# Performance work log

Measured on AMD Instinct MI355X. Metric: run time of the kernel, lower is better.

## Reference

```python
import jax, jax.numpy as jnp
import numpy as np

S, B, IN, OUT = 32, 256, 1024, 1024

def setup_inputs() -> dict:
    key = jax.random.key(0)
    ks = jax.random.split(key, 7)
    return {
        "input": jax.random.normal(ks[0], (S, B, IN), dtype=jnp.float32),
        "weight_mu": jax.random.normal(ks[1], (OUT, IN), dtype=jnp.float32) * 0.1,
        "weight_rho": jax.random.normal(ks[2], (OUT, IN), dtype=jnp.float32) - 3.0,
        "bias_mu": jax.random.normal(ks[3], (OUT,), dtype=jnp.float32) * 0.1,
        "bias_rho": jax.random.normal(ks[4], (OUT,), dtype=jnp.float32) - 3.0,
        "eps_w": jax.random.normal(ks[5], (S, OUT, IN), dtype=jnp.float32),
        "eps_b": jax.random.normal(ks[6], (S, OUT), dtype=jnp.float32),
    }

def reference(input, weight_mu, weight_rho, bias_mu, bias_rho, eps_w, eps_b):
    # sigma = log(1 + exp(rho))  (softplus)
    weight_sigma = jax.nn.softplus(weight_rho)              # (out, in)
    bias_sigma = jax.nn.softplus(bias_rho)                  # (out,)
    # reparameterized samples: (S, out, in) and (S, out)
    weight = weight_mu[None, :, :] + weight_sigma[None, :, :] * eps_w
    bias = bias_mu[None, :] + bias_sigma[None, :] * eps_b
    # batch_linear: per-sample x @ W^T + b
    out = jnp.einsum('sbi,soi->sbo', input, weight) + bias[:, None, :]
    return out
```

## Files before the change

### kernel.cpp

```cpp
#include <hip/hip_runtime.h>
#include <hip/hip_bf16.h>

constexpr int kS   = 32;
constexpr int kB   = 256;
constexpr int kIN  = 1024;
constexpr int kOUT = 1024;
constexpr int BM   = 256;
constexpr int BN   = 64;
constexpr int BK   = 32;
constexpr int NT   = kIN / BK;

typedef __bf16 v8bf __attribute__((ext_vector_type(8)));
typedef float  v4f  __attribute__((ext_vector_type(4)));

__device__ __forceinline__ float softplus_f(float x) {
    return fmaxf(x, 0.0f) + log1pf(expf(-fabsf(x)));
}
__device__ __forceinline__ unsigned int bfbits(float x) {
    __bf16 h = (__bf16)x;
    unsigned short u;
    __builtin_memcpy(&u, &h, 2);
    return (unsigned int)u;
}
__device__ __forceinline__ float asf(unsigned int u) {
    float f; __builtin_memcpy(&f, &u, 4); return f;
}

__global__ void sigma_pack(const float* __restrict__ mu, const float* __restrict__ rho,
                           uint4* __restrict__ ms) {
    int gid = blockIdx.x * blockDim.x + threadIdx.x;
    float4 m = reinterpret_cast<const float4*>(mu)[gid];
    float4 r = reinterpret_cast<const float4*>(rho)[gid];
    uint4 o;
    o.x = bfbits(m.x) | (bfbits(softplus_f(r.x)) << 16);
    o.y = bfbits(m.y) | (bfbits(softplus_f(r.y)) << 16);
    o.z = bfbits(m.z) | (bfbits(softplus_f(r.z)) << 16);
    o.w = bfbits(m.w) | (bfbits(softplus_f(r.w)) << 16);
    ms[gid] = o;
}

__global__ void xcast_kernel(const float* __restrict__ X, __bf16* __restrict__ Xb) {
    size_t i = ((size_t)blockIdx.x * blockDim.x + threadIdx.x) * 8;
    float4 a = *reinterpret_cast<const float4*>(X + i);
    float4 b = *reinterpret_cast<const float4*>(X + i + 4);
    v8bf r;
    r[0] = (__bf16)a.x; r[1] = (__bf16)a.y; r[2] = (__bf16)a.z; r[3] = (__bf16)a.w;
    r[4] = (__bf16)b.x; r[5] = (__bf16)b.y; r[6] = (__bf16)b.z; r[7] = (__bf16)b.w;
    *reinterpret_cast<v8bf*>(Xb + i) = r;
}

#define GLDS16(g, l) __builtin_amdgcn_global_load_lds(                      \
    (const __attribute__((address_space(1))) void*)(g),                     \
    (__attribute__((address_space(3))) void*)(l), 16, 0, 0)

template<bool XBF>
__global__ __launch_bounds__(512, 2) void dv_main(
        const void* __restrict__ Xv,
        const unsigned int* __restrict__ MS,
        const float* __restrict__ Ew,
        const float* __restrict__ Bmu,
        const float* __restrict__ Brho,
        const float* __restrict__ Eb,
        float* __restrict__ O)
{
    __shared__ __attribute__((aligned(16))) __bf16       Xs[3][BM * BK];
    __shared__ __attribute__((aligned(16))) float        Epb[3][BN * BK];
    __shared__ __attribute__((aligned(16))) unsigned int Msb[3][BN * BK];

    const int tid = threadIdx.x, bb = blockIdx.x;
    const int xcd = bb & 7;
    const int jj  = bb >> 3;
    const int s   = (xcd << 2) | (jj & 3);
    const int o_base = (jj >> 2) * BN;

    const int lane = tid & 63, wv = tid >> 6;
    const int mwv = wv >> 1, nwv = wv & 1;
    const int lr = lane & 15, kg = lane >> 4;

    const __bf16* Xbase = (const __bf16*)Xv + (size_t)s * kB * kIN;
    const int erow = wv * 8 + (lane >> 3);
    const int ec16 = (lane & 7) ^ ((lane >> 3) & 7);
    const float*        Ebase = Ew + ((size_t)s * kOUT + o_base + erow) * kIN + ec16 * 4;
    const unsigned int* Mbase = MS + (size_t)(o_base + erow) * kIN + ec16 * 4;
    const float* Xgf = (const float*)Xv + ((size_t)s * kB + mwv * 64 + lr) * kIN + kg * 8;

    auto STAGE = [&](int t, int bf) {
        if constexpr (XBF) {
            #pragma unroll
            for (int q = 0; q < 2; ++q) {
                int row = wv * 32 + q * 16 + (lane >> 2);
                int qg  = ((lane & 3) - (row >> 2)) & 3;
                GLDS16(Xbase + (size_t)row * kIN + t * BK + qg * 8,
                       &Xs[bf][(wv * 32 + q * 16) * BK]);
            }
        }
        GLDS16(Ebase + t * BK, &Epb[bf][wv * 256]);
        GLDS16(Mbase + t * BK, &Msb[bf][wv * 256]);
    };

    v4f acc[4][2] = {};

    STAGE(0, 0);
    STAGE(1, 1);

    for (int t = 0; t < NT; ++t) {
        const int bf = t % 3;

        if (t < NT - 1) {
            if constexpr (XBF)
                asm volatile("s_waitcnt vmcnt(4) lgkmcnt(0)" ::: "memory");
            else
                asm volatile("s_waitcnt vmcnt(2) lgkmcnt(0)" ::: "memory");
        } else {
            asm volatile("s_waitcnt vmcnt(0) lgkmcnt(0)" ::: "memory");
        }
        __builtin_amdgcn_s_barrier();

        if (t + 2 < NT) STAGE(t + 2, (t + 2) % 3);

        v8bf a[4];
        if constexpr (XBF) {
            #pragma unroll
            for (int mf = 0; mf < 4; ++mf) {
                int row = mwv * 64 + mf * 16 + lr;
                int ql  = (kg + (row >> 2)) & 3;
                a[mf] = *reinterpret_cast<const v8bf*>(&Xs[bf][row * BK + ql * 8]);
            }
        } else {
            #pragma unroll
            for (int mf = 0; mf < 4; ++mf) {
                const float* xp = Xgf + (size_t)mf * 16 * kIN + t * BK;
                float4 x0 = *reinterpret_cast<const float4*>(xp);
                float4 x1 = *reinterpret_cast<const float4*>(xp + 4);
                v8bf tt;
                tt[0] = (__bf16)x0.x; tt[1] = (__bf16)x0.y;
                tt[2] = (__bf16)x0.z; tt[3] = (__bf16)x0.w;
                tt[4] = (__bf16)x1.x; tt[5] = (__bf16)x1.y;
                tt[6] = (__bf16)x1.z; tt[7] = (__bf16)x1.w;
                a[mf] = tt;
            }
        }

        v8bf b[2];
        const char* eb = (const char*)&Epb[bf][0];
        const char* mb = (const char*)&Msb[bf][0];
        #pragma unroll
        for (int nf = 0; nf < 2; ++nf) {
            int r  = nwv * 32 + nf * 16 + lr;
            int o0 = (r * 128 + kg * 32) ^ ((r & 7) << 4);
            float4 e0 = *reinterpret_cast<const float4*>(eb + o0);
            float4 e1 = *reinterpret_cast<const float4*>(eb + (o0 ^ 16));
            uint4  p0 = *reinterpret_cast<const uint4*>(mb + o0);
            uint4  p1 = *reinterpret_cast<const uint4*>(mb + (o0 ^ 16));
            b[nf][0] = (__bf16)fmaf(asf(p0.x & 0xffff0000u), e0.x, asf(p0.x << 16));
            b[nf][1] = (__bf16)fmaf(asf(p0.y & 0xffff0000u), e0.y, asf(p0.y << 16));
            b[nf][2] = (__bf16)fmaf(asf(p0.z & 0xffff0000u), e0.z, asf(p0.z << 16));
            b[nf][3] = (__bf16)fmaf(asf(p0.w & 0xffff0000u), e0.w, asf(p0.w << 16));
            b[nf][4] = (__bf16)fmaf(asf(p1.x & 0xffff0000u), e1.x, asf(p1.x << 16));
            b[nf][5] = (__bf16)fmaf(asf(p1.y & 0xffff0000u), e1.y, asf(p1.y << 16));
            b[nf][6] = (__bf16)fmaf(asf(p1.z & 0xffff0000u), e1.z, asf(p1.z << 16));
            b[nf][7] = (__bf16)fmaf(asf(p1.w & 0xffff0000u), e1.w, asf(p1.w << 16));
        }

        #pragma unroll
        for (int mf = 0; mf < 4; ++mf)
            #pragma unroll
            for (int nf = 0; nf < 2; ++nf)
                acc[mf][nf] = __builtin_amdgcn_mfma_f32_16x16x32_bf16(
                    a[mf], b[nf], acc[mf][nf], 0, 0, 0);
    }

    float bias[2];
    #pragma unroll
    for (int nf = 0; nf < 2; ++nf) {
        int o = o_base + nwv * 32 + nf * 16 + lr;
        bias[nf] = fmaf(softplus_f(Brho[o]), Eb[(size_t)s * kOUT + o], Bmu[o]);
    }
    #pragma unroll
    for (int mf = 0; mf < 4; ++mf) {
        #pragma unroll
        for (int rr = 0; rr < 4; ++rr) {
            int mrow = mwv * 64 + mf * 16 + kg * 4 + rr;
            float* orow = O + ((size_t)s * kB + mrow) * kOUT + o_base + nwv * 32;
            #pragma unroll
            for (int nf = 0; nf < 2; ++nf)
                __builtin_nontemporal_store(acc[mf][nf][rr] + bias[nf],
                                            orow + nf * 16 + lr);
        }
    }
}

extern "C" void kernel_launch(void* const* d_in, const int* in_sizes, int n_in,
                              void* d_out, int out_size, void* d_ws, size_t ws_size,
                              hipStream_t stream) {
    const float* input = (const float*)d_in[0];
    const float* w_mu  = (const float*)d_in[1];
    const float* w_rho = (const float*)d_in[2];
    const float* b_mu  = (const float*)d_in[3];
    const float* b_rho = (const float*)d_in[4];
    const float* eps_w = (const float*)d_in[5];
    const float* eps_b = (const float*)d_in[6];
    float* out = (float*)d_out;

    const size_t ms_bytes  = (size_t)kOUT * kIN * 4;
    const size_t xbf_bytes = (size_t)kS * kB * kIN * sizeof(__bf16);
    const bool use_xbf = ws_size >= ms_bytes + xbf_bytes;

    unsigned int* ms = (unsigned int*)d_ws;
    __bf16* xbf = (__bf16*)((char*)d_ws + ms_bytes);

    sigma_pack<<<dim3((kOUT * kIN) / (256 * 4)), 256, 0, stream>>>(w_mu, w_rho, (uint4*)ms);

    dim3 grid(kS * (kOUT / BN));
    if (use_xbf) {
        xcast_kernel<<<dim3((size_t)kS * kB * kIN / (256 * 8)), 256, 0, stream>>>(input, xbf);
        dv_main<true><<<grid, 512, 0, stream>>>(xbf, ms, eps_w, b_mu, b_rho, eps_b, out);
    } else {
        dv_main<false><<<grid, 512, 0, stream>>>(input, ms, eps_w, b_mu, b_rho, eps_b, out);
    }
}
```

Before: 298.0 us.

## Split weight sampling into a pre-pass producing tiled bf16 weights for GEMM

Adds a wmat kernel that computes the sampled weights mu + sigma*eps once, stored as bf16 in a pre-swizzled per-tile layout. The GEMM then loads ready bf16 weight tiles instead of fp32 eps and packed mu/sigma, removing conversion math from the inner loop, and raises occupancy to 4 blocks per SM. The cost is an extra write and read of a 64MB intermediate. A naive fallback kernel replaces the fp32-input path when workspace is insufficient.

After: 302.1 us. Within noise of the previous version (+1.4%).

```diff
diff --git a/kernel.cpp b/kernel.cpp
--- a/kernel.cpp
+++ b/kernel.cpp
@@ -5,11 +5,11 @@
 constexpr int kB   = 256;
 constexpr int kIN  = 1024;
 constexpr int kOUT = 1024;
-constexpr int BM   = 256;
 constexpr int BN   = 64;
 constexpr int BK   = 32;
 constexpr int NT   = kIN / BK;
 
+typedef __bf16 v4bf __attribute__((ext_vector_type(4)));
 typedef __bf16 v8bf __attribute__((ext_vector_type(8)));
 typedef float  v4f  __attribute__((ext_vector_type(4)));
 
@@ -49,53 +49,84 @@
     *reinterpret_cast<v8bf*>(Xb + i) = r;
 }
 
+__global__ __launch_bounds__(256, 4) void wmat(
+        const unsigned int* __restrict__ MS,
+        const float* __restrict__ Ew,
+        __bf16* __restrict__ Wp)
+{
+    const int bb  = blockIdx.x;
+    const int s   = bb & 31;
+    const int rr  = bb >> 5;
+    const int ot  = rr >> 2;
+    const int q   = rr & 3;
+    const int tid = threadIdx.x;
+
+    const float*        Eg = Ew + ((size_t)s * kOUT + ot * 64) * kIN;
+    const unsigned int* Mg = MS + (size_t)(ot * 64) * kIN;
+    char* Wt = (char*)(Wp + ((size_t)(s * 16 + ot) * NT) * 2048);
+
+    #pragma unroll 4
+    for (int i = tid; i < 16 * 256; i += 256) {
+        int row = q * 16 + (i >> 8);
+        int k   = (i & 255) * 4;
+        float4 e = *reinterpret_cast<const float4*>(Eg + (size_t)row * kIN + k);
+        uint4  p = *reinterpret_cast<const uint4*>(Mg + (size_t)row * kIN + k);
+        v4bf w;
+        w[0] = (__bf16)fmaf(asf(p.x & 0xffff0000u), e.x, asf(p.x << 16));
+        w[1] = (__bf16)fmaf(asf(p.y & 0xffff0000u), e.y, asf(p.y << 16));
+        w[2] = (__bf16)fmaf(asf(p.z & 0xffff0000u), e.z, asf(p.z << 16));
+        w[3] = (__bf16)fmaf(asf(p.w & 0xffff0000u), e.w, asf(p.w << 16));
+        int t    = k >> 5;
+        int slot = ((k >> 3) & 3) ^ ((row >> 1) & 3);
+        *reinterpret_cast<v4bf*>(Wt + t * 4096 + row * 64 + slot * 16 + (k & 7) * 2) = w;
+    }
+}
+
 #define GLDS16(g, l) __builtin_amdgcn_global_load_lds(                      \
     (const __attribute__((address_space(1))) void*)(g),                     \
     (__attribute__((address_space(3))) void*)(l), 16, 0, 0)
-
-template<bool XBF>
-__global__ __launch_bounds__(512, 2) void dv_main(
-        const void* __restrict__ Xv,
-        const unsigned int* __restrict__ MS,
-        const float* __restrict__ Ew,
+#define GLDS4(g, l) __builtin_amdgcn_global_load_lds(                       \
+    (const __attribute__((address_space(1))) void*)(g),                     \
+    (__attribute__((address_space(3))) void*)(l), 4, 0, 0)
+
+__global__ __launch_bounds__(512, 4) void dv_gemm(
+        const __bf16* __restrict__ Xb,
+        const __bf16* __restrict__ Wp,
         const float* __restrict__ Bmu,
         const float* __restrict__ Brho,
         const float* __restrict__ Eb,
         float* __restrict__ O)
 {
-    __shared__ __attribute__((aligned(16))) __bf16       Xs[3][BM * BK];
-    __shared__ __attribute__((aligned(16))) float        Epb[3][BN * BK];
-    __shared__ __attribute__((aligned(16))) unsigned int Msb[3][BN * BK];
+    __shared__ __attribute__((aligned(16))) __bf16 Xs[3][kB * BK];
+    __shared__ __attribute__((aligned(16))) __bf16 Ws[3][BN * BK];
 
     const int tid = threadIdx.x, bb = blockIdx.x;
     const int xcd = bb & 7;
     const int jj  = bb >> 3;
     const int s   = (xcd << 2) | (jj & 3);
-    const int o_base = (jj >> 2) * BN;
+    const int ot  = jj >> 2;
+    const int o_base = ot * BN;
 
     const int lane = tid & 63, wv = tid >> 6;
     const int mwv = wv >> 1, nwv = wv & 1;
     const int lr = lane & 15, kg = lane >> 4;
 
-    const __bf16* Xbase = (const __bf16*)Xv + (size_t)s * kB * kIN;
-    const int erow = wv * 8 + (lane >> 3);
-    const int ec16 = (lane & 7) ^ ((lane >> 3) & 7);
-    const float*        Ebase = Ew + ((size_t)s * kOUT + o_base + erow) * kIN + ec16 * 4;
-    const unsigned int* Mbase = MS + (size_t)(o_base + erow) * kIN + ec16 * 4;
-    const float* Xgf = (const float*)Xv + ((size_t)s * kB + mwv * 64 + lr) * kIN + kg * 8;
+    const __bf16* Xbase = Xb + (size_t)s * kB * kIN;
+    const char*   Wbase = (const char*)(Wp + ((size_t)(s * 16 + ot) * NT) * 2048);
+
+    const int xrow = wv * 32 + (lane >> 2);
+    const int xq0  = ((lane & 3) - (xrow >> 2)) & 3;
+    const int xq1  = ((lane & 3) - ((xrow + 16) >> 2)) & 3;
 
     auto STAGE = [&](int t, int bf) {
-        if constexpr (XBF) {
-            #pragma unroll
-            for (int q = 0; q < 2; ++q) {
-                int row = wv * 32 + q * 16 + (lane >> 2);
-                int qg  = ((lane & 3) - (row >> 2)) & 3;
-                GLDS16(Xbase + (size_t)row * kIN + t * BK + qg * 8,
-                       &Xs[bf][(wv * 32 + q * 16) * BK]);
-            }
-        }
-        GLDS16(Ebase + t * BK, &Epb[bf][wv * 256]);
-        GLDS16(Mbase + t * BK, &Msb[bf][wv * 256]);
+        GLDS16(Xbase + (size_t)xrow * kIN + t * BK + xq0 * 8,
+               &Xs[bf][(wv * 32) * BK]);
+        GLDS16(Xbase + (size_t)(xrow + 16) * kIN + t * BK + xq1 * 8,
+               &Xs[bf][(wv * 32 + 16) * BK]);
+        const char* wt = Wbase + t * 4096 + wv * 512;
+        char*       wl = (char*)&Ws[bf][0] + wv * 512;
+        GLDS4(wt + lane * 4,       wl);
+        GLDS4(wt + 256 + lane * 4, wl + 256);
     };
 
     v4f acc[4][2] = {};
@@ -106,60 +137,28 @@
     for (int t = 0; t < NT; ++t) {
         const int bf = t % 3;
 
-        if (t < NT - 1) {
-            if constexpr (XBF)
-                asm volatile("s_waitcnt vmcnt(4) lgkmcnt(0)" ::: "memory");
-            else
-                asm volatile("s_waitcnt vmcnt(2) lgkmcnt(0)" ::: "memory");
-        } else {
+        if (t < NT - 1)
+            asm volatile("s_waitcnt vmcnt(4) lgkmcnt(0)" ::: "memory");
+        else
             asm volatile("s_waitcnt vmcnt(0) lgkmcnt(0)" ::: "memory");
+        __builtin_amdgcn_s_barrier();
+
+        if (t + 2 < NT) STAGE(t + 2, (t + 2) % 3);
+
+        v8bf a[4];
+        #pragma unroll
+        for (int mf = 0; mf < 4; ++mf) {
+            int row = mwv * 64 + mf * 16 + lr;
+            int ql  = (kg + (row >> 2)) & 3;
+            a[mf] = *reinterpret_cast<const v8bf*>(&Xs[bf][row * BK + ql * 8]);
         }
-        __builtin_amdgcn_s_barrier();
-
-        if (t + 2 < NT) STAGE(t + 2, (t + 2) % 3);
-
-        v8bf a[4];
-        if constexpr (XBF) {
-            #pragma unroll
-            for (int mf = 0; mf < 4; ++mf) {
-                int row = mwv * 64 + mf * 16 + lr;
-                int ql  = (kg + (row >> 2)) & 3;
-                a[mf] = *reinterpret_cast<const v8bf*>(&Xs[bf][row * BK + ql * 8]);
-            }
-        } else {
-            #pragma unroll
-            for (int mf = 0; mf < 4; ++mf) {
-                const float* xp = Xgf + (size_t)mf * 16 * kIN + t * BK;
-                float4 x0 = *reinterpret_cast<const float4*>(xp);
-                float4 x1 = *reinterpret_cast<const float4*>(xp + 4);
-                v8bf tt;
-                tt[0] = (__bf16)x0.x; tt[1] = (__bf16)x0.y;
-                tt[2] = (__bf16)x0.z; tt[3] = (__bf16)x0.w;
-                tt[4] = (__bf16)x1.x; tt[5] = (__bf16)x1.y;
-                tt[6] = (__bf16)x1.z; tt[7] = (__bf16)x1.w;
-                a[mf] = tt;
-            }
-        }
-
         v8bf b[2];
-        const char* eb = (const char*)&Epb[bf][0];
-        const char* mb = (const char*)&Msb[bf][0];
         #pragma unroll
         for (int nf = 0; nf < 2; ++nf) {
-            int r  = nwv * 32 + nf * 16 + lr;
-            int o0 = (r * 128 + kg * 32) ^ ((r & 7) << 4);
-            float4 e0 = *reinterpret_cast<const float4*>(eb + o0);
-            float4 e1 = *reinterpret_cast<const float4*>(eb + (o0 ^ 16));
-            uint4  p0 = *reinterpret_cast<const uint4*>(mb + o0);
-            uint4  p1 = *reinterpret_cast<const uint4*>(mb + (o0 ^ 16));
-            b[nf][0] = (__bf16)fmaf(asf(p0.x & 0xffff0000u), e0.x, asf(p0.x << 16));
-            b[nf][1] = (__bf16)fmaf(asf(p0.y & 0xffff0000u), e0.y, asf(p0.y << 16));
-            b[nf][2] = (__bf16)fmaf(asf(p0.z & 0xffff0000u), e0.z, asf(p0.z << 16));
-            b[nf][3] = (__bf16)fmaf(asf(p0.w & 0xffff0000u), e0.w, asf(p0.w << 16));
-            b[nf][4] = (__bf16)fmaf(asf(p1.x & 0xffff0000u), e1.x, asf(p1.x << 16));
-            b[nf][5] = (__bf16)fmaf(asf(p1.y & 0xffff0000u), e1.y, asf(p1.y << 16));
-            b[nf][6] = (__bf16)fmaf(asf(p1.z & 0xffff0000u), e1.z, asf(p1.z << 16));
-            b[nf][7] = (__bf16)fmaf(asf(p1.w & 0xffff0000u), e1.w, asf(p1.w << 16));
+            int row  = nwv * 32 + nf * 16 + lr;
+            int slot = kg ^ ((row >> 1) & 3);
+            b[nf] = *reinterpret_cast<const v8bf*>(
+                (const char*)&Ws[bf][0] + row * 64 + slot * 16);
         }
 
         #pragma unroll
@@ -188,6 +187,24 @@
                                             orow + nf * 16 + lr);
         }
     }
+}
+
+__global__ void dv_naive(const float* __restrict__ X, const float* __restrict__ Wmu,
+                         const float* __restrict__ Wrho, const float* __restrict__ Bmu,
+                         const float* __restrict__ Brho, const float* __restrict__ Ew,
+                         const float* __restrict__ Eb, float* __restrict__ O) {
+    size_t gid = (size_t)blockIdx.x * blockDim.x + threadIdx.x;
+    int o = gid % kOUT;
+    int b = (gid / kOUT) % kB;
+    int s = gid / ((size_t)kOUT * kB);
+    const float* x = X + ((size_t)s * kB + b) * kIN;
+    const float* e = Ew + ((size_t)s * kOUT + o) * kIN;
+    const float* wm = Wmu + (size_t)o * kIN;
+    const float* wr = Wrho + (size_t)o * kIN;
+    float acc = 0.f;
+    for (int k = 0; k < kIN; ++k)
+        acc += x[k] * fmaf(softplus_f(wr[k]), e[k], wm[k]);
+    O[gid] = acc + fmaf(softplus_f(Brho[o]), Eb[(size_t)s * kOUT + o], Bmu[o]);
 }
 
 extern "C" void kernel_launch(void* const* d_in, const int* in_sizes, int n_in,
@@ -204,18 +221,20 @@
 
     const size_t ms_bytes  = (size_t)kOUT * kIN * 4;
     const size_t xbf_bytes = (size_t)kS * kB * kIN * sizeof(__bf16);
-    const bool use_xbf = ws_size >= ms_bytes + xbf_bytes;
+    const size_t wp_bytes  = (size_t)kS * kOUT * kIN * sizeof(__bf16);
+
+    if (ws_size < ms_bytes + xbf_bytes + wp_bytes) {
+        dv_naive<<<dim3((size_t)kS * kB * kOUT / 256), 256, 0, stream>>>(
+            input, w_mu, w_rho, b_mu, b_rho, eps_w, eps_b, out);
+        return;
+    }
 
     unsigned int* ms = (unsigned int*)d_ws;
     __bf16* xbf = (__bf16*)((char*)d_ws + ms_bytes);
+    __bf16* wp  = (__bf16*)((char*)d_ws + ms_bytes + xbf_bytes);
 
     sigma_pack<<<dim3((kOUT * kIN) / (256 * 4)), 256, 0, stream>>>(w_mu, w_rho, (uint4*)ms);
-
-    dim3 grid(kS * (kOUT / BN));
-    if (use_xbf) {
-        xcast_kernel<<<dim3((size_t)kS * kB * kIN / (256 * 8)), 256, 0, stream>>>(input, xbf);
-        dv_main<true><<<grid, 512, 0, stream>>>(xbf, ms, eps_w, b_mu, b_rho, eps_b, out);
-    } else {
-        dv_main<false><<<grid, 512, 0, stream>>>(input, ms, eps_w, b_mu, b_rho, eps_b, out);
-    }
-}
+    xcast_kernel<<<dim3((size_t)kS * kB * kIN / (256 * 8)), 256, 0, stream>>>(input, xbf);
+    wmat<<<dim3(2048), 256, 0, stream>>>(ms, eps_w, wp);
+    dv_gemm<<<dim3(kS * (kOUT / BN)), 512, 0, stream>>>(xbf, wp, b_mu, b_rho, eps_b, out);
+}
```
